# Kernel optimization log

Hardware: AMD Instinct MI355X
Metric: run time of the kernel (lower is better)

## Reference

```python
import jax, jax.numpy as jnp
import numpy as np

B, S, DIM, H = 2, 2048, 1024, 16
DH = DIM // H            # 64
G = DH // 4              # 16 quaternion groups per head
IQ = DIM // 4            # 256
ROPE_BASE = 10000.0
SCALE = DH ** -0.5


def qlinear(x, wr, wi, wj, wk, b):
    # x: [B,S,4*IQ]; strided quaternion components, exact combo from QuaternionLinear.forward
    xr, xi, xj, xk = x[..., 0::4], x[..., 1::4], x[..., 2::4], x[..., 3::4]
    o_r = xr @ wr.T - xi @ wi.T - xj @ wj.T - xk @ wk.T
    o_i = xi @ wr.T + xr @ wi.T + xk @ wk.T - xj @ wj.T
    o_j = xj @ wr.T - xk @ wk.T + xr @ wj.T + xi @ wi.T
    o_k = xk @ wr.T + xj @ wj.T - xi @ wi.T + xr @ wk.T
    out = jnp.stack([o_r, o_i, o_j, o_k], axis=-1).reshape(x.shape[:-1] + (-1,))
    return out + b


def qrope(x):
    # x: [B,H,S,DH]; left quaternion multiply u(theta) \otimes q, axis_mode='cycle'
    b, h, s, dh = x.shape
    g = dh // 4
    xq = x.reshape(b, h, s, g, 4)
    t = jnp.arange(s, dtype=x.dtype)
    inv = 1.0 / (ROPE_BASE ** (jnp.arange(g, dtype=x.dtype) / g))
    ang = t[:, None] * inv[None, :]            # [S,G]
    cos, sin = jnp.cos(ang), jnp.sin(ang)
    gi = jnp.arange(g)
    ax_i = (gi % 3 == 0).astype(x.dtype)
    ax_j = (gi % 3 == 1).astype(x.dtype)
    ax_k = (gi % 3 == 2).astype(x.dtype)
    ur, ui, uj, uk = cos, sin * ax_i, sin * ax_j, sin * ax_k   # [S,G] broadcast over [B,H,S,G]
    xr, xi, xj, xk = xq[..., 0], xq[..., 1], xq[..., 2], xq[..., 3]
    pr = ur * xr - ui * xi - uj * xj - uk * xk
    pi = ur * xi + ui * xr + uj * xk - uk * xj
    pj = ur * xj - ui * xk + uj * xr + uk * xi
    pk = ur * xk + ui * xj - uj * xi + uk * xr
    return jnp.stack([pr, pi, pj, pk], axis=-1).reshape(b, h, s, dh)


def setup_inputs() -> dict:
    key = jax.random.key(0)
    ks = jax.random.split(key, 24)
    x = jax.random.normal(ks[0], (B, S, DIM), dtype=jnp.float32)
    # causal mask: True = masked
    mask = jnp.broadcast_to(jnp.triu(jnp.ones((S, S), dtype=bool), k=1), (B, S, S))
    inp = {"x": x, "mask": mask}
    i = 1
    for proj in ("q", "k", "v", "o"):
        for comp in ("wr", "wi", "wj", "wk"):
            inp[f"{proj}_{comp}"] = jax.random.normal(ks[i], (IQ, IQ), dtype=jnp.float32) * 0.02
            i += 1
        inp[f"{proj}_b"] = jnp.zeros((DIM,), dtype=jnp.float32)
    return inp


def reference(x, mask,
              q_wr, q_wi, q_wj, q_wk, q_b,
              k_wr, k_wi, k_wj, k_wk, k_b,
              v_wr, v_wi, v_wj, v_wk, v_b,
              o_wr, o_wi, o_wj, o_wk, o_b):
    b, s, dm = x.shape
    q = qlinear(x, q_wr, q_wi, q_wj, q_wk, q_b).reshape(b, s, H, DH).transpose(0, 2, 1, 3)
    k = qlinear(x, k_wr, k_wi, k_wj, k_wk, k_b).reshape(b, s, H, DH).transpose(0, 2, 1, 3)
    v = qlinear(x, v_wr, v_wi, v_wj, v_wk, v_b).reshape(b, s, H, DH).transpose(0, 2, 1, 3)
    q, k = qrope(q), qrope(k)
    scores = jnp.einsum('bhsd,bhtd->bhst', q, k) * SCALE
    scores = jnp.where(mask[:, None, :, :], -jnp.inf, scores)
    a = jax.nn.softmax(scores, axis=-1)
    out = jnp.einsum('bhst,bhtd->bhsd', a, v).transpose(0, 2, 1, 3).reshape(b, s, dm)
    return qlinear(out, o_wr, o_wi, o_wj, o_wk, o_b)
```

## Files before the change

kernel.cpp:

```cpp
#include <hip/hip_runtime.h>
#include <stdint.h>

typedef unsigned short u16;
typedef unsigned int   u32;

#define NB   2
#define NS   2048
#define NDIM 1024
#define NH   16
#define NDH  64
#define QSCALE 0.18033688011112042f

typedef __bf16 bf16x8 __attribute__((ext_vector_type(8)));
typedef float  f32x4  __attribute__((ext_vector_type(4)));

#define MFMA_BF16(a,b,c) __builtin_amdgcn_mfma_f32_16x16x32_bf16((a),(b),(c),0,0,0)

#define XBF_OFF   (256)
#define WD_OFF    (XBF_OFF  + 8*1024*1024)
#define BIAS_OFF  (WD_OFF   + 8*1024*1024)
#define QB_OFF    (BIAS_OFF + 16384)
#define KB_OFF    (QB_OFF   + 8*1024*1024)
#define VT_OFF    (KB_OFF   + 8*1024*1024)
#define OP_OFF    (VT_OFF   + 8*1024*1024)
#define LP_OFF    (OP_OFF   + 16*1024*1024)

__device__ __forceinline__ float bf2f(u16 h){
  union { u32 u; float f; } v; v.u = ((u32)h) << 16; return v.f;
}
__device__ __forceinline__ u16 f2bf(float f){
  union { float f; u32 u; } v; v.f = f;
  u32 r = (v.u >> 16) & 1u;
  return (u16)((v.u + 0x7fffu + r) >> 16);
}
__device__ __forceinline__ float load_val(const void* p, int i, int isbf){
  return isbf ? bf2f(((const u16*)p)[i]) : ((const float*)p)[i];
}
__device__ __forceinline__ void gl_lds16(const u16* g, u16* l){
  __builtin_amdgcn_global_load_lds(
      (__attribute__((address_space(1))) void*)(uintptr_t)g,
      (__attribute__((address_space(3))) void*)(uintptr_t)l,
      16, 0, 0);
}

__global__ void detect_kernel(const u16* __restrict__ x, int* __restrict__ flag){
  __shared__ int cnt;
  if (threadIdx.x == 0) cnt = 0;
  __syncthreads();
  int ok = 0;
  int base = threadIdx.x * 16;
  for (int i = base; i < base + 16; ++i){
    u16 h = x[i];
    int e = (h >> 7) & 0xFF;
    if ((e > 96 && e < 158) || ((h & 0x7FFF) == 0)) ok++;
  }
  atomicAdd(&cnt, ok);
  __syncthreads();
  if (threadIdx.x == 0) *flag = (cnt > 3600) ? 1 : 0;
}

__global__ void conv_x_kernel(const void* __restrict__ xin, u16* __restrict__ xbf,
                              const int* __restrict__ flag){
  int isbf = *flag;
  int t = blockIdx.x * 256 + threadIdx.x;
  if (isbf){
    ((uint4*)xbf)[t] = ((const uint4*)xin)[t];
  } else {
    const float4* f4 = (const float4*)xin;
    float4 a = f4[2*t], b = f4[2*t+1];
    ushort4 lo = { f2bf(a.x), f2bf(a.y), f2bf(a.z), f2bf(a.w) };
    ushort4 hi = { f2bf(b.x), f2bf(b.y), f2bf(b.z), f2bf(b.w) };
    ((ushort4*)xbf)[2*t]   = lo;
    ((ushort4*)xbf)[2*t+1] = hi;
  }
}

struct QPtrs { const void* w[16]; const void* b[4]; };

__global__ void build_w_kernel(QPtrs ptrs, u16* __restrict__ wd,
                               float* __restrict__ biasf, const int* __restrict__ flag){
  int isbf = *flag;
  int idx = blockIdx.x * 256 + threadIdx.x;
  int n = idx & 255, m = (idx >> 8) & 255, c = (idx >> 16) & 3, p = idx >> 18;
  int src = m * 256 + n;
  float vr = load_val(ptrs.w[p*4+0], src, isbf);
  float vi = load_val(ptrs.w[p*4+1], src, isbf);
  float vj = load_val(ptrs.w[p*4+2], src, isbf);
  float vk = load_val(ptrs.w[p*4+3], src, isbf);
  float o0, o1, o2, o3;
  switch (c){
    case 0:  o0 = vr; o1 = -vi; o2 = -vj; o3 = -vk; break;
    case 1:  o0 = vi; o1 =  vr; o2 = -vj; o3 =  vk; break;
    case 2:  o0 = vj; o1 =  vi; o2 =  vr; o3 = -vk; break;
    default: o0 = vk; o1 = -vi; o2 =  vj; o3 =  vr; break;
  }
  ushort4 sv = { f2bf(o0), f2bf(o1), f2bf(o2), f2bf(o3) };
  *(ushort4*)&wd[(size_t)p * 1048576 + (size_t)(4*m + c) * 1024 + 4*n] = sv;
  if (idx < 4096){
    int pp = idx >> 10, oo = idx & 1023;
    biasf[idx] = load_val(ptrs.b[pp], oo, isbf);
  }
}

__global__ __launch_bounds__(256)
void gemm_qkv_kernel(const u16* __restrict__ A, const u16* __restrict__ Bw,
                     const float* __restrict__ bias,
                     u16* __restrict__ qb, u16* __restrict__ kb, u16* __restrict__ vt){
  __shared__ u16 sA[3][128 * 32];
  __shared__ u16 sB[3][128 * 32];
  int tid = threadIdx.x, w = tid >> 6, lane = tid & 63, quad = lane >> 4, l16 = lane & 15;
  int n0 = blockIdx.x * 128, m0 = blockIdx.y * 128;

  f32x4 acc[4][4];
#pragma unroll
  for (int i = 0; i < 4; ++i)
#pragma unroll
    for (int j = 0; j < 4; ++j) acc[i][j] = (f32x4){0.f, 0.f, 0.f, 0.f};

  int cp = lane & 3, rl = lane >> 2;
  int gc = (cp ^ ((rl >> 1) & 3)) * 8;
  const u16* ga = A  + (size_t)(m0 + w*16 + rl) * 1024 + gc;
  const u16* gb = Bw + (size_t)(n0 + w*16 + rl) * 1024 + gc;
  int ldo = w * 512 + lane * 8;
  int xorv = ((l16 >> 1) & 3) * 8;
  int mw = (w & 1) * 64, nw = (w >> 1) * 64;

  auto stage = [&](int k0, int b){
#pragma unroll
    for (int i = 0; i < 2; ++i){
      gl_lds16(ga + (size_t)i * 65536 + k0, &sA[b][ldo + i * 2048]);
      gl_lds16(gb + (size_t)i * 65536 + k0, &sB[b][ldo + i * 2048]);
    }
  };

  stage(0, 0);
  stage(32, 1);
  asm volatile("s_waitcnt vmcnt(4)" ::: "memory");
  __builtin_amdgcn_s_barrier();

  int bcur = 0, bnxt = 2;
  for (int it = 0; it < 32; ++it){
    if (it < 30) stage((it + 2) * 32, bnxt);
    const u16* cA = sA[bcur];
    const u16* cB = sB[bcur];
    bf16x8 af[4], bfr[4];
#pragma unroll
    for (int mt = 0; mt < 4; ++mt)
      af[mt] = *(const bf16x8*)&cA[(mw + mt*16 + l16) * 32 + (quad*8 ^ xorv)];
#pragma unroll
    for (int nt = 0; nt < 4; ++nt)
      bfr[nt] = *(const bf16x8*)&cB[(nw + nt*16 + l16) * 32 + (quad*8 ^ xorv)];
#pragma unroll
    for (int mt = 0; mt < 4; ++mt)
#pragma unroll
      for (int nt = 0; nt < 4; ++nt)
        acc[mt][nt] = MFMA_BF16(af[mt], bfr[nt], acc[mt][nt]);

    if (it < 30) asm volatile("s_waitcnt vmcnt(4)" ::: "memory");
    else         asm volatile("s_waitcnt vmcnt(0)" ::: "memory");
    __builtin_amdgcn_s_barrier();
    bcur = (bcur == 2) ? 0 : bcur + 1;
    bnxt = (bnxt == 2) ? 0 : bnxt + 1;
  }

  int proj = n0 >> 10;
  if (proj == 2){
#pragma unroll
    for (int mt = 0; mt < 4; ++mt){
      int row = m0 + mw + mt*16 + quad*4;
      int b = row >> 11, seq0 = row & 2047;
#pragma unroll
      for (int nt = 0; nt < 4; ++nt){
        int col = n0 + nw + nt*16 + l16;
        int o = col & 1023, h = o >> 6, d = o & 63;
        float bv = bias[col];
        ushort4 pv = { f2bf(acc[mt][nt][0] + bv), f2bf(acc[mt][nt][1] + bv),
                       f2bf(acc[mt][nt][2] + bv), f2bf(acc[mt][nt][3] + bv) };
        *(ushort4*)&vt[((size_t)((b*16 + h) * 64 + d)) * 2048 + seq0] = pv;
      }
    }
  } else {
    float sc = (proj == 0) ? QSCALE : 1.0f;
    u16* dst = proj ? kb : qb;
    int c = l16 & 3;
#pragma unroll
    for (int nt = 0; nt < 4; ++nt){
      int col = n0 + nw + nt*16 + l16;
      int o = col & 1023, h = o >> 6, d = o & 63;
      int g = d >> 2;
      int ax = g % 3;
      int mask = ax + 1;
      int tbl = (ax == 0) ? 0xA : (ax == 1 ? 0x6 : 0xC);
      float sgn = ((tbl >> c) & 1) ? 1.f : -1.f;
      float inv = __builtin_amdgcn_exp2f(-(float)g * 0.8304820237218405f);
      float bv = bias[col];
#pragma unroll
      for (int mt = 0; mt < 4; ++mt){
        int row0 = m0 + mw + mt*16 + quad*4;
        int b = row0 >> 11, s0 = row0 & 2047;
        size_t obase = ((size_t)((b*16 + h) * 2048 + s0)) * 64 + d;
#pragma unroll
        for (int r = 0; r < 4; ++r){
          float v = acc[mt][nt][r] + bv;
          float vp = __shfl_xor(v, mask);
          float ang = (float)(s0 + r) * inv;
          float co = __cosf(ang) * sc;
          float si = __sinf(ang) * sc * sgn;
          dst[obase + (size_t)r * 64] = f2bf(co * v + si * vp);
        }
      }
    }
  }
}

__global__ __launch_bounds__(256)
void gemm_o_kernel(const u16* __restrict__ A, const u16* __restrict__ Bw,
                   const float* __restrict__ bias, void* __restrict__ dout,
                   const int* __restrict__ flag){
  __shared__ u16 sA[3][64 * 32];
  __shared__ u16 sB[3][128 * 32];
  int tid = threadIdx.x, w = tid >> 6, lane = tid & 63, quad = lane >> 4, l16 = lane & 15;
  int n0 = blockIdx.x * 128, m0 = blockIdx.y * 64;

  f32x4 acc[2][4];
#pragma unroll
  for (int i = 0; i < 2; ++i)
#pragma unroll
    for (int j = 0; j < 4; ++j) acc[i][j] = (f32x4){0.f, 0.f, 0.f, 0.f};

  int cp = lane & 3, rl = lane >> 2;
  int gc = (cp ^ ((rl >> 1) & 3)) * 8;
  int xorv = ((l16 >> 1) & 3) * 8;
  int mw = (w & 1) * 32, nw = (w >> 1) * 64;

  auto stage = [&](int k0, int b){
#pragma unroll
    for (int i = 0; i < 3; ++i){
      int ch = w * 3 + i;
      int lr = (ch < 4 ? ch : ch - 4) * 16 + rl;
      int eo = (ch < 4 ? ch : ch - 4) * 512 + lane * 8;
      if (ch < 4) gl_lds16(A  + (size_t)(m0 + lr) * 1024 + k0 + gc, &sA[b][eo]);
      else        gl_lds16(Bw + (size_t)(n0 + lr) * 1024 + k0 + gc, &sB[b][eo]);
    }
  };

  stage(0, 0);
  stage(32, 1);
  asm volatile("s_waitcnt vmcnt(3)" ::: "memory");
  __builtin_amdgcn_s_barrier();

  int bcur = 0, bnxt = 2;
  for (int it = 0; it < 32; ++it){
    if (it < 30) stage((it + 2) * 32, bnxt);
    const u16* cA = sA[bcur];
    const u16* cB = sB[bcur];
    bf16x8 af[2], bfr[4];
#pragma unroll
    for (int mt = 0; mt < 2; ++mt)
      af[mt] = *(const bf16x8*)&cA[(mw + mt*16 + l16) * 32 + (quad*8 ^ xorv)];
#pragma unroll
    for (int nt = 0; nt < 4; ++nt)
      bfr[nt] = *(const bf16x8*)&cB[(nw + nt*16 + l16) * 32 + (quad*8 ^ xorv)];
#pragma unroll
    for (int mt = 0; mt < 2; ++mt)
#pragma unroll
      for (int nt = 0; nt < 4; ++nt)
        acc[mt][nt] = MFMA_BF16(af[mt], bfr[nt], acc[mt][nt]);

    if (it < 30) asm volatile("s_waitcnt vmcnt(3)" ::: "memory");
    else         asm volatile("s_waitcnt vmcnt(0)" ::: "memory");
    __builtin_amdgcn_s_barrier();
    bcur = (bcur == 2) ? 0 : bcur + 1;
    bnxt = (bnxt == 2) ? 0 : bnxt + 1;
  }

  int isbf = *flag;
#pragma unroll
  for (int mt = 0; mt < 2; ++mt){
    int row = m0 + mw + mt*16 + quad*4;
#pragma unroll
    for (int nt = 0; nt < 4; ++nt){
      int col = n0 + nw + nt*16 + l16;
      float bv = bias[col];
#pragma unroll
      for (int r = 0; r < 4; ++r){
        float val = acc[mt][nt][r] + bv;
        size_t addr = (size_t)(row + r) * 1024 + col;
        if (isbf) ((u16*)dout)[addr] = f2bf(val);
        else      ((float*)dout)[addr] = val;
      }
    }
  }
}

#define SPT 20

__global__ __launch_bounds__(256, 2)
void attn_kernel(const u16* __restrict__ Q, const u16* __restrict__ K,
                 const u16* __restrict__ Vt, u16* __restrict__ OP,
                 float* __restrict__ LP){
  __shared__ u16 sK[2][4096];
  __shared__ u16 sPT[4][64 * SPT];
  int bh  = blockIdx.x;
  int spl = blockIdx.y;
  int tid = threadIdx.x, w = tid >> 6, lane = tid & 63, quad = lane >> 4, l16 = lane & 15;
  size_t kbase = (size_t)bh * 2048 * 64;
  size_t vbase = (size_t)bh * 64 * 2048;
  u16* spw = &sPT[w][0];

  auto stage = [&](int kt, int b){
    int kcol = kt * 64;
#pragma unroll
    for (int p = 0; p < 2; ++p){
      int slot = w*128 + p*64 + lane;
      int row = slot >> 3, dc = (slot & 7) ^ (row & 7);
      gl_lds16(K + kbase + (size_t)(kcol + row) * 64 + dc*8, &sK[b][(w*128 + p*64) * 8]);
    }
  };

  for (int item = 0; item < 2; ++item){
    int qt = item ? (int)blockIdx.z : 15 - (int)blockIdx.z;
    int rowbase = qt * 128 + w * 32;

    bf16x8 qf[2][2];
#pragma unroll
    for (int g = 0; g < 2; ++g)
#pragma unroll
      for (int kc = 0; kc < 2; ++kc)
        qf[g][kc] = *(const bf16x8*)(Q + kbase + (size_t)(rowbase + g*16 + l16) * 64 + kc*32 + quad*8);

    f32x4 oaccT[2][4];
    float lsum[2][4];
#pragma unroll
    for (int g = 0; g < 2; ++g)
#pragma unroll
      for (int i = 0; i < 4; ++i){ oaccT[g][i] = (f32x4){0.f,0.f,0.f,0.f}; lsum[g][i] = 0.f; }

    int kt0 = spl ? (qt + 1) : 0;
    int ntiles = qt + 1;

    stage(kt0, 0);
    for (int i = 0; i < ntiles; ++i){
      int kcol = (kt0 + i) * 64;
      __syncthreads();
      if (i + 1 < ntiles) stage(kt0 + i + 1, (i + 1) & 1);
      const u16* bK = sK[i & 1];

      if (kcol <= rowbase + 31){
        bf16x8 vf[4][2];
#pragma unroll
        for (int dn = 0; dn < 4; ++dn)
#pragma unroll
          for (int kc = 0; kc < 2; ++kc)
            vf[dn][kc] = *(const bf16x8*)(Vt + vbase + (size_t)(dn*16 + l16) * 2048
                                          + kcol + kc*32 + quad*8);
        bf16x8 bk[2][4];
#pragma unroll
        for (int kc = 0; kc < 2; ++kc)
#pragma unroll
          for (int nt = 0; nt < 4; ++nt){
            int rw = nt*16 + l16;
            int ch = ((kc*4 + quad) ^ (rw & 7)) * 8;
            bk[kc][nt] = *(const bf16x8*)&bK[rw*64 + ch];
          }
#pragma unroll
        for (int g = 0; g < 2; ++g){
          int G0 = rowbase + g*16;
          if (kcol <= G0 + 15){
            f32x4 sacc[4];
#pragma unroll
            for (int nt = 0; nt < 4; ++nt) sacc[nt] = (f32x4){0.f,0.f,0.f,0.f};
#pragma unroll
            for (int kc = 0; kc < 2; ++kc)
#pragma unroll
              for (int nt = 0; nt < 4; ++nt)
                sacc[nt] = MFMA_BF16(qf[g][kc], bk[kc][nt], sacc[nt]);

            if (kcol + 63 > G0){
#pragma unroll
              for (int nt = 0; nt < 4; ++nt){
                int col = kcol + nt*16 + l16;
                ushort4 pv;
#pragma unroll
                for (int r = 0; r < 4; ++r){
                  int row = G0 + quad*4 + r;
                  float pp = (col <= row) ? __builtin_amdgcn_exp2f(sacc[nt][r]) : 0.f;
                  lsum[g][r] += pp;
                  ((u16*)&pv)[r] = f2bf(pp);
                }
                *(ushort4*)&spw[(nt*16 + l16) * SPT + quad*4] = pv;
              }
            } else {
#pragma unroll
              for (int nt = 0; nt < 4; ++nt){
                ushort4 pv;
#pragma unroll
                for (int r = 0; r < 4; ++r){
                  float pp = __builtin_amdgcn_exp2f(sacc[nt][r]);
                  lsum[g][r] += pp;
                  ((u16*)&pv)[r] = f2bf(pp);
                }
                *(ushort4*)&spw[(nt*16 + l16) * SPT + quad*4] = pv;
              }
            }
#pragma unroll
            for (int kc = 0; kc < 2; ++kc){
              bf16x8 pf;
#pragma unroll
              for (int j = 0; j < 8; ++j)
                pf[j] = ((const __bf16*)spw)[(kc*32 + quad*8 + j) * SPT + l16];
#pragma unroll
              for (int dn = 0; dn < 4; ++dn)
                oaccT[g][dn] = MFMA_BF16(vf[dn][kc], pf, oaccT[g][dn]);
            }
          }
        }
      }
    }

    float* scr = (float*)spw;
#pragma unroll
    for (int g = 0; g < 2; ++g)
#pragma unroll
      for (int r = 0; r < 4; ++r){
        float l = lsum[g][r];
        l += __shfl_xor(l, 1); l += __shfl_xor(l, 2);
        l += __shfl_xor(l, 4); l += __shfl_xor(l, 8);
        if (l16 == 0) scr[g*16 + quad*4 + r] = l;
      }
    float lrow[2];
#pragma unroll
    for (int g = 0; g < 2; ++g) lrow[g] = scr[g*16 + l16];

    size_t obase = ((size_t)(spl*32 + bh)) * 2048;
#pragma unroll
    for (int g = 0; g < 2; ++g){
      int row = rowbase + g*16 + l16;
      if (quad == 0) LP[obase + row] = lrow[g];
#pragma unroll
      for (int dn = 0; dn < 4; ++dn){
        ushort4 ov = { f2bf(oaccT[g][dn][0]), f2bf(oaccT[g][dn][1]),
                       f2bf(oaccT[g][dn][2]), f2bf(oaccT[g][dn][3]) };
        *(ushort4*)&OP[(obase + row) * 64 + dn*16 + quad*4] = ov;
      }
    }

    __syncthreads();
  }
}

__global__ void combine_kernel(const u16* __restrict__ OP, const float* __restrict__ LP,
                               u16* __restrict__ Ab){
  int idx = blockIdx.x * 256 + threadIdx.x;
  int dc = idx & 7, s = (idx >> 3) & 2047, bh = idx >> 14;
  size_t r0 = (size_t)bh * 2048 + s, r1 = (size_t)(32 + bh) * 2048 + s;
  float invl = 1.f / (LP[r0] + LP[r1]);
  union { uint4 v; u16 h[8]; } a0, a1; ushort4 o[2];
  a0.v = *(const uint4*)&OP[r0 * 64 + dc*8];
  a1.v = *(const uint4*)&OP[r1 * 64 + dc*8];
#pragma unroll
  for (int p = 0; p < 2; ++p)
#pragma unroll
    for (int j = 0; j < 4; ++j)
      ((u16*)&o[p])[j] = f2bf((bf2f(a0.h[p*4+j]) + bf2f(a1.h[p*4+j])) * invl);
  int b = bh >> 4, h = bh & 15;
  u16* dst = &Ab[((size_t)(b*2048 + s)) * 1024 + h*64 + dc*8];
  *(ushort4*)dst = o[0];
  *(ushort4*)(dst + 4) = o[1];
}

extern "C" void kernel_launch(void* const* d_in, const int* in_sizes, int n_in,
                              void* d_out, int out_size, void* d_ws, size_t ws_size,
                              hipStream_t stream){
  (void)in_sizes; (void)n_in; (void)out_size; (void)ws_size;
  char* ws = (char*)d_ws;
  int*   flag  = (int*)ws;
  u16*   Xbf   = (u16*)(ws + XBF_OFF);
  u16*   Wd    = (u16*)(ws + WD_OFF);
  float* biasf = (float*)(ws + BIAS_OFF);
  u16*   Qb    = (u16*)(ws + QB_OFF);
  u16*   Kb    = (u16*)(ws + KB_OFF);
  u16*   Vt    = (u16*)(ws + VT_OFF);
  u16*   OP    = (u16*)(ws + OP_OFF);
  float* LP    = (float*)(ws + LP_OFF);
  u16*   Ab    = Xbf;

  detect_kernel<<<1, 256, 0, stream>>>((const u16*)d_in[0], flag);
  conv_x_kernel<<<2048, 256, 0, stream>>>(d_in[0], Xbf, flag);

  QPtrs ptrs;
  for (int p = 0; p < 4; ++p){
    for (int wi = 0; wi < 4; ++wi) ptrs.w[p*4 + wi] = d_in[2 + p*5 + wi];
    ptrs.b[p] = d_in[2 + p*5 + 4];
  }
  build_w_kernel<<<4096, 256, 0, stream>>>(ptrs, Wd, biasf, flag);

  gemm_qkv_kernel<<<dim3(24, 32), 256, 0, stream>>>(Xbf, Wd, biasf, Qb, Kb, Vt);
  attn_kernel<<<dim3(32, 2, 8), 256, 0, stream>>>(Qb, Kb, Vt, OP, LP);
  combine_kernel<<<2048, 256, 0, stream>>>(OP, LP, Ab);
  gemm_o_kernel<<<dim3(8, 64), 256, 0, stream>>>(Ab, Wd + 3*1048576, biasf + 3072,
                                                 d_out, flag);
}
```

Measured before the change: 243.2 us.

## Fuse prep kernels into one and fold split-KV combine into output GEMM

Merges detect, x conversion and weight build into a single prep kernel, where every block redoes the dtype detection locally. It also removes the combine kernel by having the output GEMM load the two partial attention outputs and LSE sums directly. The GEMM normalises them in registers and writes the result to LDS. This saves two launches and the Ab round trip through memory. In exchange the GEMM A-tile path becomes register-staged with a full vmcnt(0) wait and only double buffering instead of a 3-stage async pipeline, and the combine arithmetic is repeated across the 8 column blocks.

```diff
diff --git a/kernel.cpp b/kernel.cpp
--- a/kernel.cpp
+++ b/kernel.cpp
@@ -43,44 +43,47 @@
       16, 0, 0);
 }
 
-__global__ void detect_kernel(const u16* __restrict__ x, int* __restrict__ flag){
+struct QPtrs { const void* w[16]; const void* b[4]; };
+
+__global__ void prep_kernel(const void* __restrict__ xin, QPtrs ptrs,
+                            u16* __restrict__ xbf, u16* __restrict__ wd,
+                            float* __restrict__ biasf, int* __restrict__ flag){
   __shared__ int cnt;
   if (threadIdx.x == 0) cnt = 0;
   __syncthreads();
-  int ok = 0;
-  int base = threadIdx.x * 16;
-  for (int i = base; i < base + 16; ++i){
-    u16 h = x[i];
-    int e = (h >> 7) & 0xFF;
-    if ((e > 96 && e < 158) || ((h & 0x7FFF) == 0)) ok++;
-  }
-  atomicAdd(&cnt, ok);
+  {
+    const uint4* xv = (const uint4*)xin;
+    uint4 v0 = xv[threadIdx.x * 2], v1 = xv[threadIdx.x * 2 + 1];
+    const u16* hh = (const u16*)&v0;
+    int ok = 0;
+#pragma unroll
+    for (int i = 0; i < 16; ++i){
+      u16 h = (i < 8) ? hh[i] : ((const u16*)&v1)[i - 8];
+      int e = (h >> 7) & 0xFF;
+      if ((e > 96 && e < 158) || ((h & 0x7FFF) == 0)) ok++;
+    }
+    atomicAdd(&cnt, ok);
+  }
   __syncthreads();
-  if (threadIdx.x == 0) *flag = (cnt > 3600) ? 1 : 0;
-}
-
-__global__ void conv_x_kernel(const void* __restrict__ xin, u16* __restrict__ xbf,
-                              const int* __restrict__ flag){
-  int isbf = *flag;
-  int t = blockIdx.x * 256 + threadIdx.x;
-  if (isbf){
-    ((uint4*)xbf)[t] = ((const uint4*)xin)[t];
-  } else {
-    const float4* f4 = (const float4*)xin;
-    float4 a = f4[2*t], b = f4[2*t+1];
-    ushort4 lo = { f2bf(a.x), f2bf(a.y), f2bf(a.z), f2bf(a.w) };
-    ushort4 hi = { f2bf(b.x), f2bf(b.y), f2bf(b.z), f2bf(b.w) };
-    ((ushort4*)xbf)[2*t]   = lo;
-    ((ushort4*)xbf)[2*t+1] = hi;
-  }
-}
-
-struct QPtrs { const void* w[16]; const void* b[4]; };
-
-__global__ void build_w_kernel(QPtrs ptrs, u16* __restrict__ wd,
-                               float* __restrict__ biasf, const int* __restrict__ flag){
-  int isbf = *flag;
+  int isbf = (cnt > 3600) ? 1 : 0;
+  if (blockIdx.x == 0 && threadIdx.x == 0) *flag = isbf;
+
   int idx = blockIdx.x * 256 + threadIdx.x;
+
+  if (blockIdx.x < 2048){
+    int t = idx;
+    if (isbf){
+      ((uint4*)xbf)[t] = ((const uint4*)xin)[t];
+    } else {
+      const float4* f4 = (const float4*)xin;
+      float4 a = f4[2*t], b = f4[2*t+1];
+      ushort4 lo = { f2bf(a.x), f2bf(a.y), f2bf(a.z), f2bf(a.w) };
+      ushort4 hi = { f2bf(b.x), f2bf(b.y), f2bf(b.z), f2bf(b.w) };
+      ((ushort4*)xbf)[2*t]   = lo;
+      ((ushort4*)xbf)[2*t+1] = hi;
+    }
+  }
+
   int n = idx & 255, m = (idx >> 8) & 255, c = (idx >> 16) & 3, p = idx >> 18;
   int src = m * 256 + n;
   float vr = load_val(ptrs.w[p*4+0], src, isbf);
@@ -214,11 +217,11 @@
 }
 
 __global__ __launch_bounds__(256)
-void gemm_o_kernel(const u16* __restrict__ A, const u16* __restrict__ Bw,
-                   const float* __restrict__ bias, void* __restrict__ dout,
-                   const int* __restrict__ flag){
-  __shared__ u16 sA[3][64 * 32];
-  __shared__ u16 sB[3][128 * 32];
+void gemm_o_kernel(const u16* __restrict__ OP, const float* __restrict__ LP,
+                   const u16* __restrict__ Bw, const float* __restrict__ bias,
+                   void* __restrict__ dout, const int* __restrict__ flag){
+  __shared__ u16 sA[2][64 * 32];
+  __shared__ u16 sB[2][128 * 32];
   int tid = threadIdx.x, w = tid >> 6, lane = tid & 63, quad = lane >> 4, l16 = lane & 15;
   int n0 = blockIdx.x * 128, m0 = blockIdx.y * 64;
 
@@ -233,27 +236,57 @@
   int xorv = ((l16 >> 1) & 3) * 8;
   int mw = (w & 1) * 32, nw = (w >> 1) * 64;
 
-  auto stage = [&](int k0, int b){
+  uint4 la0[3], la1[3];
+  float lp0[3], lp1[3];
+
+  auto issue_stage = [&](int k0, int b){
 #pragma unroll
     for (int i = 0; i < 3; ++i){
       int ch = w * 3 + i;
       int lr = (ch < 4 ? ch : ch - 4) * 16 + rl;
-      int eo = (ch < 4 ? ch : ch - 4) * 512 + lane * 8;
-      if (ch < 4) gl_lds16(A  + (size_t)(m0 + lr) * 1024 + k0 + gc, &sA[b][eo]);
-      else        gl_lds16(Bw + (size_t)(n0 + lr) * 1024 + k0 + gc, &sB[b][eo]);
+      if (ch < 4){
+        int row = m0 + lr;
+        int bb = row >> 11, ss = row & 2047;
+        int c0 = k0 + gc, hh = c0 >> 6, d0 = c0 & 63;
+        size_t r0 = ((size_t)(bb*16 + hh)) * 2048 + ss;
+        size_t r1 = r0 + (size_t)32 * 2048;
+        la0[i] = *(const uint4*)&OP[r0 * 64 + d0];
+        la1[i] = *(const uint4*)&OP[r1 * 64 + d0];
+        lp0[i] = LP[r0];
+        lp1[i] = LP[r1];
+      } else {
+        int eo = (ch - 4) * 512 + lane * 8;
+        gl_lds16(Bw + (size_t)(n0 + lr) * 1024 + k0 + gc, &sB[b][eo]);
+      }
     }
   };
-
-  stage(0, 0);
-  stage(32, 1);
-  asm volatile("s_waitcnt vmcnt(3)" ::: "memory");
-  __builtin_amdgcn_s_barrier();
-
-  int bcur = 0, bnxt = 2;
+  auto write_stage = [&](int b){
+#pragma unroll
+    for (int i = 0; i < 3; ++i){
+      int ch = w * 3 + i;
+      if (ch < 4){
+        int eo = ch * 512 + lane * 8;
+        float il = 1.f / (lp0[i] + lp1[i]);
+        const u16* h0 = (const u16*)&la0[i];
+        const u16* h1 = (const u16*)&la1[i];
+        union { uint4 v; u16 h[8]; } o;
+#pragma unroll
+        for (int j = 0; j < 8; ++j)
+          o.h[j] = f2bf((bf2f(h0[j]) + bf2f(h1[j])) * il);
+        *(uint4*)&sA[b][eo] = o.v;
+      }
+    }
+  };
+
+  issue_stage(0, 0);
+  asm volatile("s_waitcnt vmcnt(0)" ::: "memory");
+  write_stage(0);
+  __syncthreads();
+
   for (int it = 0; it < 32; ++it){
-    if (it < 30) stage((it + 2) * 32, bnxt);
-    const u16* cA = sA[bcur];
-    const u16* cB = sB[bcur];
+    if (it < 31) issue_stage((it + 1) * 32, (it + 1) & 1);
+    const u16* cA = sA[it & 1];
+    const u16* cB = sB[it & 1];
     bf16x8 af[2], bfr[4];
 #pragma unroll
     for (int mt = 0; mt < 2; ++mt)
@@ -267,11 +300,11 @@
       for (int nt = 0; nt < 4; ++nt)
         acc[mt][nt] = MFMA_BF16(af[mt], bfr[nt], acc[mt][nt]);
 
-    if (it < 30) asm volatile("s_waitcnt vmcnt(3)" ::: "memory");
-    else         asm volatile("s_waitcnt vmcnt(0)" ::: "memory");
-    __builtin_amdgcn_s_barrier();
-    bcur = (bcur == 2) ? 0 : bcur + 1;
-    bnxt = (bnxt == 2) ? 0 : bnxt + 1;
+    if (it < 31){
+      asm volatile("s_waitcnt vmcnt(0)" ::: "memory");
+      write_stage((it + 1) & 1);
+    }
+    __syncthreads();
   }
 
   int isbf = *flag;
@@ -447,26 +480,6 @@
 
     __syncthreads();
   }
-}
-
-__global__ void combine_kernel(const u16* __restrict__ OP, const float* __restrict__ LP,
-                               u16* __restrict__ Ab){
-  int idx = blockIdx.x * 256 + threadIdx.x;
-  int dc = idx & 7, s = (idx >> 3) & 2047, bh = idx >> 14;
-  size_t r0 = (size_t)bh * 2048 + s, r1 = (size_t)(32 + bh) * 2048 + s;
-  float invl = 1.f / (LP[r0] + LP[r1]);
-  union { uint4 v; u16 h[8]; } a0, a1; ushort4 o[2];
-  a0.v = *(const uint4*)&OP[r0 * 64 + dc*8];
-  a1.v = *(const uint4*)&OP[r1 * 64 + dc*8];
-#pragma unroll
-  for (int p = 0; p < 2; ++p)
-#pragma unroll
-    for (int j = 0; j < 4; ++j)
-      ((u16*)&o[p])[j] = f2bf((bf2f(a0.h[p*4+j]) + bf2f(a1.h[p*4+j])) * invl);
-  int b = bh >> 4, h = bh & 15;
-  u16* dst = &Ab[((size_t)(b*2048 + s)) * 1024 + h*64 + dc*8];
-  *(ushort4*)dst = o[0];
-  *(ushort4*)(dst + 4) = o[1];
 }
 
 extern "C" void kernel_launch(void* const* d_in, const int* in_sizes, int n_in,
@@ -483,21 +496,16 @@
   u16*   Vt    = (u16*)(ws + VT_OFF);
   u16*   OP    = (u16*)(ws + OP_OFF);
   float* LP    = (float*)(ws + LP_OFF);
-  u16*   Ab    = Xbf;
-
-  detect_kernel<<<1, 256, 0, stream>>>((const u16*)d_in[0], flag);
-  conv_x_kernel<<<2048, 256, 0, stream>>>(d_in[0], Xbf, flag);
 
   QPtrs ptrs;
   for (int p = 0; p < 4; ++p){
     for (int wi = 0; wi < 4; ++wi) ptrs.w[p*4 + wi] = d_in[2 + p*5 + wi];
     ptrs.b[p] = d_in[2 + p*5 + 4];
   }
-  build_w_kernel<<<4096, 256, 0, stream>>>(ptrs, Wd, biasf, flag);
-
+
+  prep_kernel<<<4096, 256, 0, stream>>>(d_in[0], ptrs, Xbf, Wd, biasf, flag);
   gemm_qkv_kernel<<<dim3(24, 32), 256, 0, stream>>>(Xbf, Wd, biasf, Qb, Kb, Vt);
   attn_kernel<<<dim3(32, 2, 8), 256, 0, stream>>>(Qb, Kb, Vt, OP, LP);
-  combine_kernel<<<2048, 256, 0, stream>>>(OP, LP, Ab);
-  gemm_o_kernel<<<dim3(8, 64), 256, 0, stream>>>(Ab, Wd + 3*1048576, biasf + 3072,
+  gemm_o_kernel<<<dim3(8, 64), 256, 0, stream>>>(OP, LP, Wd + 3*1048576, biasf + 3072,
                                                  d_out, flag);
 }
```

After: 262.7 us. 1.08x slower.
